# Kernel tuning notes

Hardware: AMD Instinct MI355X
Metric: run time of the kernel (lower is better)

The kernel has to match this reference:

```python
import jax, jax.numpy as jnp
import numpy as np

K = 20          # num neighbors (init kwarg k)
BN_EPS = 1e-5   # PyTorch BatchNorm default eps


def setup_inputs() -> dict:
    key = jax.random.key(0)
    k1, k2 = jax.random.split(key, 2)
    x = jax.random.normal(k1, (8, 64, 4096), dtype=jnp.float32)       # (b, d, n)
    w = jax.random.normal(k2, (64, 128), dtype=jnp.float32) * 0.05    # Conv2d 1x1: (out=64, in=2*64)
    gamma = jnp.ones((64,), jnp.float32)    # BatchNorm1d weight
    beta = jnp.zeros((64,), jnp.float32)    # BatchNorm1d bias
    return {"x": x, "w": w, "gamma": gamma, "beta": beta}


def reference(x, w, gamma, beta):
    # x: (b, d, n)
    xt = jnp.swapaxes(x, 1, 2)                       # (b, n, d)
    # kNN via pairwise squared euclidean distance (same ordering as torch.cdist)
    sq = jnp.sum(xt * xt, axis=-1)                   # (b, n)
    d2 = sq[:, :, None] + sq[:, None, :] - 2.0 * jnp.einsum('bnd,bmd->bnm', xt, xt)
    _, idx = jax.lax.top_k(-d2, K)                   # (b, n, K) smallest distances
    # gather neighbor features: (b, n, K, d)
    nb = jax.vmap(lambda pts, i: pts[i])(xt, idx)
    ctr = xt[:, :, None, :]                          # (b, n, 1, d)
    # edge feature = concat([neighbor - x, x]) -> (b, n, K, 2d)
    feat = jnp.concatenate([nb - ctr, jnp.broadcast_to(ctr, nb.shape)], axis=-1)
    # 1x1 conv (no bias) then max over neighbors
    h = jnp.max(jnp.einsum('bnkc,oc->bnko', feat, w), axis=2)   # (b, n, out)
    # BatchNorm1d (training mode: batch statistics over (b, n), biased var)
    mean = jnp.mean(h, axis=(0, 1))
    var = jnp.mean((h - mean) ** 2, axis=(0, 1))
    hn = (h - mean) / jnp.sqrt(var + BN_EPS) * gamma + beta
    out = jax.nn.gelu(hn, approximate=False)         # exact GELU (PyTorch default)
    return jnp.swapaxes(out, 1, 2)                   # (b, out, n)
```

## Files before the change

### kernel.cpp

```cpp
#include <hip/hip_runtime.h>

#define BIGF 3.402823466e38f

typedef __attribute__((ext_vector_type(8))) short bf16x8;
typedef __attribute__((ext_vector_type(4))) float f32x4;

__device__ __forceinline__ void gload_lds16(const float* g, float* lds) {
  __builtin_amdgcn_global_load_lds((const __attribute__((address_space(1))) void*)g,
                                   (__attribute__((address_space(3))) void*)lds, 16, 0, 0);
}
__device__ __forceinline__ void gload_lds16u(const unsigned short* g, unsigned short* lds) {
  __builtin_amdgcn_global_load_lds((const __attribute__((address_space(1))) void*)g,
                                   (__attribute__((address_space(3))) void*)lds, 16, 0, 0);
}

__device__ __forceinline__ unsigned short bf16_rne(float f) {
  unsigned int u = __float_as_uint(f);
  return (unsigned short)((u + 0x7fffu + ((u >> 16) & 1u)) >> 16);
}

__global__ __launch_bounds__(256) void k1_pre(const float* __restrict__ x, const float* __restrict__ w,
                                              float* __restrict__ sq, float* __restrict__ y,
                                              float* __restrict__ delta, unsigned short* __restrict__ xhl) {
  __shared__ __align__(16) float xt[64][68];
  __shared__ __align__(16) float ws[128][64];
  const int t = threadIdx.x;
  const int bid = blockIdx.x;
  const int b = bid >> 6;
  const int n0 = (bid & 63) << 6;
  const float* xb = x + (size_t)b * 64 * 4096;

#pragma unroll
  for (int rep = 0; rep < 16; ++rep) {
    int id = rep * 256 + t;
    int d = id >> 6, n = id & 63;
    xt[n][d] = xb[(size_t)d * 4096 + n0 + n];
  }
#pragma unroll
  for (int rep = 0; rep < 32; ++rep) {
    int id = rep * 256 + t;
    int u = id >> 6, dd = id & 63;
    ws[u][dd] = w[(u & 63) * 128 + ((u >> 6) << 6) + dd];
  }
  __syncthreads();

  {
    const int p = t >> 2;
    const int cg = t & 3;
    uint4* orow = (uint4*)xhl + ((size_t)(b << 12) + n0 + p) * 16;
#pragma unroll
    for (int cc = 0; cc < 4; ++cc) {
      const int c = cg * 4 + cc;
      const int kb = (c & 7) * 8;
      const bool lohalf = (c >= 8);
      unsigned int pk[4];
#pragma unroll
      for (int j2 = 0; j2 < 4; ++j2) {
        unsigned short u0, u1;
#pragma unroll
        for (int e = 0; e < 2; ++e) {
          const float xv = xt[p][kb + j2 * 2 + e];
          unsigned short h = bf16_rne(xv);
          unsigned short r;
          if (!lohalf) r = h;
          else r = bf16_rne(xv - __uint_as_float(((unsigned int)h) << 16));
          if (e == 0) u0 = r; else u1 = r;
        }
        pk[j2] = (unsigned int)u0 | ((unsigned int)u1 << 16);
      }
      uint4 v;
      v.x = pk[0]; v.y = pk[1]; v.z = pk[2]; v.w = pk[3];
      orow[c ^ (p & 7)] = v;
    }
  }

  const int p = t & 63;
  const int oc = t >> 6;
  float accy[16], accz[16];
#pragma unroll
  for (int j = 0; j < 16; ++j) { accy[j] = 0.f; accz[j] = 0.f; }

#pragma unroll 4
  for (int d4 = 0; d4 < 16; ++d4) {
    const float4 xv = *(const float4*)&xt[p][d4 * 4];
#pragma unroll
    for (int j = 0; j < 16; ++j) {
      const int o = oc * 16 + j;
      const float4 wy = *(const float4*)&ws[o][d4 * 4];
      const float4 wz = *(const float4*)&ws[o + 64][d4 * 4];
      accy[j] = fmaf(xv.x, wy.x, fmaf(xv.y, wy.y, fmaf(xv.z, wy.z, fmaf(xv.w, wy.w, accy[j]))));
      accz[j] = fmaf(xv.x, wz.x, fmaf(xv.y, wz.y, fmaf(xv.z, wz.z, fmaf(xv.w, wz.w, accz[j]))));
    }
  }

  if (oc == 0) {
    float s = 0.f;
#pragma unroll
    for (int d4 = 0; d4 < 16; ++d4) {
      const float4 v = *(const float4*)&xt[p][d4 * 4];
      s = fmaf(v.x, v.x, fmaf(v.y, v.y, fmaf(v.z, v.z, fmaf(v.w, v.w, s))));
    }
    sq[b * 4096 + n0 + p] = s;
  }

  const size_t row = ((size_t)b * 4096 + n0 + p) * 64 + oc * 16;
#pragma unroll
  for (int j4 = 0; j4 < 4; ++j4) {
    float4 yv = make_float4(accy[j4 * 4], accy[j4 * 4 + 1], accy[j4 * 4 + 2], accy[j4 * 4 + 3]);
    float4 dv = make_float4(accz[j4 * 4] - accy[j4 * 4], accz[j4 * 4 + 1] - accy[j4 * 4 + 1],
                            accz[j4 * 4 + 2] - accy[j4 * 4 + 2], accz[j4 * 4 + 3] - accy[j4 * 4 + 3]);
    *(float4*)&y[row + j4 * 4] = yv;
    *(float4*)&delta[row + j4 * 4] = dv;
  }
}

__global__ __launch_bounds__(256, 2) void k2_knn(const unsigned short* __restrict__ xhl,
                                                 const float* __restrict__ sq,
                                                 int* __restrict__ idx_out) {
  __shared__ __align__(16) float smem[4096 + 8192 + 6656 + 256];
  const int t = threadIdx.x;
  const int lane = t & 63;
  const int w = t >> 6;
  float* BsW = smem + 4096 + (w << 11);
  uint4* BsW4 = (uint4*)BsW;
  const uint4* As4 = (const uint4*)smem;
  uint2* bufL = (uint2*)(smem + 12288) + ((w << 6) + lane) * 13;
  volatile float* thrW = smem + 18944;

  const int bid = blockIdx.x;
  const int b = bid >> 6;
  const int n0 = (bid & 63) << 6;
  const int pn = lane & 15, q = lane >> 4;

  const unsigned short* xr = xhl + ((size_t)(b << 12)) * 128;
  const float* sqb = sq + (b << 12);

  thrW[t] = BIGF;

  {
    unsigned short* asu = (unsigned short*)smem;
#pragma unroll
    for (int qq = 0; qq < 4; ++qq) {
      const int kk = w * 4 + qq;
      gload_lds16u(xr + (size_t)n0 * 128 + kk * 512 + lane * 8, asu + kk * 512);
    }
  }
  __syncthreads();

  bf16x8 bfr[4][4];
#pragma unroll
  for (int nt = 0; nt < 4; ++nt)
#pragma unroll
    for (int j = 0; j < 4; ++j)
      bfr[nt][j] = *reinterpret_cast<const bf16x8*>(&As4[((nt << 4) + pn) * 16 + (((j << 2) + q) ^ (pn & 7))]);

  float kd[20];
  int ki[20];
#pragma unroll
  for (int s = 0; s < 20; ++s) { kd[s] = BIGF; ki[s] = -1; }
  const float sqn = sqb[n0 + lane];
  const int myn = lane;
  const int swz = myn & 7;
  int cnt = 0;

  auto ins = [&](float vd, int vi) {
#pragma unroll
    for (int s = 0; s < 20; ++s) {
      const float od = kd[s];
      const int oi = ki[s];
      const bool lt = vd < od;
      kd[s] = lt ? vd : od;
      ki[s] = lt ? vi : oi;
      vd = lt ? od : vd;
      vi = lt ? oi : vi;
    }
  };

  auto drain = [&]() {
#pragma unroll 1
    for (int j = 0; j < 12; ++j) {
      if (!__any(j < cnt)) break;
      if (j < cnt) {
        const uint2 e = bufL[j];
        const float dv = __uint_as_float(e.x);
        if (dv < kd[19]) ins(dv, (int)e.y);
      }
    }
    cnt = 0;
    thrW[(myn << 2) + w] = kd[19];
  };

  const f32x4 zero4 = {0.f, 0.f, 0.f, 0.f};
  f32x4 acc[4][2];
#pragma unroll
  for (int nt = 0; nt < 4; ++nt) { acc[nt][0] = zero4; acc[nt][1] = zero4; }

  for (int kt = 0; kt < 32; ++kt) {
    const int mbase = (w + 4 * kt) << 5;
    {
      unsigned short* bsu = (unsigned short*)BsW;
      const unsigned short* src = xr + (size_t)mbase * 128;
#pragma unroll
      for (int k = 0; k < 8; ++k) gload_lds16u(src + k * 512 + lane * 8, bsu + k * 512);
    }
    const f32x4 sqm0 = *(const f32x4*)&sqb[mbase + (q << 2)];
    const f32x4 sqm1 = *(const f32x4*)&sqb[mbase + 16 + (q << 2)];

    const float tw0 = thrW[(myn << 2) + 0];
    const float tw1 = thrW[(myn << 2) + 1];
    const float tw2 = thrW[(myn << 2) + 2];
    const float tw3 = thrW[(myn << 2) + 3];
    float thrS = fminf(fminf(tw0, tw1), fminf(tw2, tw3));
    thrS = fminf(thrS, kd[19]);
    const float thr2 = (thrS - sqn) + 0.0625f;

    __builtin_amdgcn_s_waitcnt(0x0F70);

#pragma unroll
    for (int mt = 0; mt < 2; ++mt) {
      bf16x8 afr[4];
#pragma unroll
      for (int j = 0; j < 4; ++j)
        afr[j] = *reinterpret_cast<const bf16x8*>(&BsW4[((mt << 4) + pn) * 16 + (((j << 2) + q) ^ (pn & 7))]);
#pragma unroll
      for (int nt = 0; nt < 4; ++nt) {
        f32x4 a = acc[nt][mt];
        a = __builtin_amdgcn_mfma_f32_16x16x32_bf16(afr[0], bfr[nt][0], a, 0, 0, 0);
        a = __builtin_amdgcn_mfma_f32_16x16x32_bf16(afr[1], bfr[nt][1], a, 0, 0, 0);
        a = __builtin_amdgcn_mfma_f32_16x16x32_bf16(afr[0], bfr[nt][2], a, 0, 0, 0);
        a = __builtin_amdgcn_mfma_f32_16x16x32_bf16(afr[1], bfr[nt][3], a, 0, 0, 0);
        a = __builtin_amdgcn_mfma_f32_16x16x32_bf16(afr[2], bfr[nt][0], a, 0, 0, 0);
        a = __builtin_amdgcn_mfma_f32_16x16x32_bf16(afr[3], bfr[nt][1], a, 0, 0, 0);
        acc[nt][mt] = a;
      }
    }

#pragma unroll
    for (int nt = 0; nt < 4; ++nt) {
#pragma unroll
      for (int mt = 0; mt < 2; ++mt) {
        const int n = (nt << 4) + pn;
        const int g = (mt << 2) + q;
        const int pc = g ^ (n & 7);
        const f32x4 sv = mt ? sqm1 : sqm0;
        f32x4 dv = sv - 2.0f * acc[nt][mt];
        *(f32x4*)&BsW[(n << 5) + (pc << 2)] = dv;
        acc[nt][mt] = zero4;
      }
    }

#pragma unroll 1
    for (int half = 0; half < 2; ++half) {
      const int cb = half << 2;
      const float4 v0 = *(const float4*)&BsW[(myn << 5) + (((cb + 0) ^ swz) << 2)];
      const float4 v1 = *(const float4*)&BsW[(myn << 5) + (((cb + 1) ^ swz) << 2)];
      const float4 v2 = *(const float4*)&BsW[(myn << 5) + (((cb + 2) ^ swz) << 2)];
      const float4 v3 = *(const float4*)&BsW[(myn << 5) + (((cb + 3) ^ swz) << 2)];
#pragma unroll
      for (int cc = 0; cc < 4; ++cc) {
        const float4 v = (cc == 0) ? v0 : (cc == 1) ? v1 : (cc == 2) ? v2 : v3;
        const int mb = mbase + ((cb + cc) << 2);
        const float mn = fminf(fminf(v.x, v.y), fminf(v.z, v.w));
        if (mn < thr2) {
          if (v.x < thr2) { bufL[cnt] = make_uint2(__float_as_uint(sqn + v.x), (unsigned)mb); cnt++; }
          if (v.y < thr2) { bufL[cnt] = make_uint2(__float_as_uint(sqn + v.y), (unsigned)(mb + 1)); cnt++; }
          if (v.z < thr2) { bufL[cnt] = make_uint2(__float_as_uint(sqn + v.z), (unsigned)(mb + 2)); cnt++; }
          if (v.w < thr2) { bufL[cnt] = make_uint2(__float_as_uint(sqn + v.w), (unsigned)(mb + 3)); cnt++; }
        }
        if (__any(cnt > 8)) drain();
      }
    }
  }
  drain();

  __syncthreads();
  float* pf = smem;
  int* pi = (int*)(smem + 5120);
#pragma unroll
  for (int s = 0; s < 20; ++s) {
    pf[(w * 20 + s) * 64 + lane] = kd[s];
    pi[(w * 20 + s) * 64 + lane] = ki[s];
  }
  __syncthreads();
  if (w == 0) {
    auto insTie = [&](float vd, int vi) {
#pragma unroll
      for (int s = 0; s < 20; ++s) {
        const float od = kd[s];
        const int oi = ki[s];
        const bool lt = (vd < od) || (vd == od && vi < oi);
        kd[s] = lt ? vd : od;
        ki[s] = lt ? vi : oi;
        vd = lt ? od : vd;
        vi = lt ? oi : vi;
      }
    };
    for (int ww = 1; ww < 4; ++ww) {
#pragma unroll 1
      for (int s = 0; s < 20; ++s) {
        const float dv = pf[(ww * 20 + s) * 64 + lane];
        const int iv = pi[(ww * 20 + s) * 64 + lane];
        if (dv < kd[19] || (dv == kd[19] && iv < ki[19])) insTie(dv, iv);
      }
    }
    int* orow = idx_out + ((size_t)(b << 12) + n0 + lane) * 20;
#pragma unroll
    for (int s = 0; s < 20; ++s) orow[s] = ki[s];
  }
}

__global__ __launch_bounds__(256) void k3_gather(const float* __restrict__ y,
                                                 const float* __restrict__ delta,
                                                 const int* __restrict__ idx,
                                                 float* __restrict__ h,
                                                 float* __restrict__ sums,
                                                 float* __restrict__ sumsq) {
  const int t = threadIdx.x;
  const int lane = t & 63;
  const int w = t >> 6;
  const int blk = blockIdx.x;
  float s1 = 0.f, s2 = 0.f;
  for (int p = 0; p < 16; ++p) {
    const int ng = blk * 64 + w * 16 + p;
    const int b = ng >> 12;
    const int* row = idx + (size_t)ng * 20;
    float mx = -BIGF;
#pragma unroll
    for (int kk = 0; kk < 20; ++kk) {
      const int nbr = row[kk];
      mx = fmaxf(mx, y[((size_t)(b << 12) + nbr) * 64 + lane]);
    }
    const float hv = mx + delta[(size_t)ng * 64 + lane];
    h[(size_t)ng * 64 + lane] = hv;
    s1 += hv;
    s2 += hv * hv;
  }
  __shared__ float r1[4][64], r2[4][64];
  r1[w][lane] = s1;
  r2[w][lane] = s2;
  __syncthreads();
  if (w == 0) {
    const float a = r1[0][lane] + r1[1][lane] + r1[2][lane] + r1[3][lane];
    const float c = r2[0][lane] + r2[1][lane] + r2[2][lane] + r2[3][lane];
    atomicAdd(&sums[lane], a);
    atomicAdd(&sumsq[lane], c);
  }
}

__global__ __launch_bounds__(256) void k4_bn(const float* __restrict__ h,
                                             const float* __restrict__ sums,
                                             const float* __restrict__ sumsq,
                                             const float* __restrict__ gamma,
                                             const float* __restrict__ beta,
                                             float* __restrict__ out) {
  __shared__ float tile[64][65];
  const int bid = blockIdx.x;
  const int b = bid >> 6;
  const int n0 = (bid & 63) << 6;
  const int t = threadIdx.x;
  const int o = t & 63;
#pragma unroll
  for (int it = 0; it < 16; ++it) {
    const int n = (t >> 6) * 16 + it;
    tile[n][o] = h[(((size_t)b << 12) + n0 + n) * 64 + o];
  }
  __syncthreads();
  const int j = t & 63;
#pragma unroll
  for (int it = 0; it < 16; ++it) {
    const int oo = (t >> 6) * 16 + it;
    const float mean = sums[oo] * (1.0f / 32768.0f);
    const float var = sumsq[oo] * (1.0f / 32768.0f) - mean * mean;
    const float sc = gamma[oo] / sqrtf(var + 1e-5f);
    const float hv = tile[j][oo];
    const float hn = (hv - mean) * sc + beta[oo];
    const float g = 0.5f * hn * (1.0f + erff(hn * 0.70710678118654752f));
    out[((size_t)(b * 64 + oo)) * 4096 + n0 + j] = g;
  }
}

extern "C" void kernel_launch(void* const* d_in, const int* in_sizes, int n_in,
                              void* d_out, int out_size, void* d_ws, size_t ws_size,
                              hipStream_t stream) {
  const float* x = (const float*)d_in[0];
  const float* w = (const float*)d_in[1];
  const float* gamma = (const float*)d_in[2];
  const float* beta = (const float*)d_in[3];
  float* out = (float*)d_out;

  float* sq_ws = (float*)d_ws;
  float* y_ws = sq_ws + 32768;
  float* delta_ws = y_ws + 2097152;
  float* h_ws = delta_ws + 2097152;
  int* idx_ws = (int*)(h_ws + 2097152);
  float* sums = (float*)(idx_ws + 655360);
  float* sumsq = sums + 64;
  unsigned short* xhl = (unsigned short*)h_ws;

  hipMemsetAsync(sums, 0, 2 * 64 * sizeof(float), stream);
  k1_pre<<<512, 256, 0, stream>>>(x, w, sq_ws, y_ws, delta_ws, xhl);
  k2_knn<<<512, 256, 0, stream>>>(xhl, sq_ws, idx_ws);
  k3_gather<<<512, 256, 0, stream>>>(y_ws, delta_ws, idx_ws, h_ws, sums, sumsq);
  k4_bn<<<512, 256, 0, stream>>>(h_ws, sums, sumsq, gamma, beta, out);
}
```

Before: 344.2 us.

## Shrink kNN LDS footprint, share threshold via atomicMin, tighten candidate margin

The per-thread candidate buffer moves from an interleaved uint2 array into two strided arrays (distance, index) that reuse the A-tile region after the B fragments are loaded into registers. This cuts k2_knn shared memory from about 19.2K floats to 12.35K floats, which may allow more resident blocks. The four per-wave threshold slots become one shared threshold per point updated with atomicMin on the float bit pattern. The threshold is refreshed after each drain, the drain trigger drops to more than 4 entries, and the pruning margin shrinks from 0.0625 to 0.001. The smaller margin prunes more aggressively, so bf16 rounding error in the distances could drop true neighbours.

Result: slower. 352.8 us (+2.5%).

```diff
diff --git a/kernel.cpp b/kernel.cpp
--- a/kernel.cpp
+++ b/kernel.cpp
@@ -5,10 +5,6 @@
 typedef __attribute__((ext_vector_type(8))) short bf16x8;
 typedef __attribute__((ext_vector_type(4))) float f32x4;
 
-__device__ __forceinline__ void gload_lds16(const float* g, float* lds) {
-  __builtin_amdgcn_global_load_lds((const __attribute__((address_space(1))) void*)g,
-                                   (__attribute__((address_space(3))) void*)lds, 16, 0, 0);
-}
 __device__ __forceinline__ void gload_lds16u(const unsigned short* g, unsigned short* lds) {
   __builtin_amdgcn_global_load_lds((const __attribute__((address_space(1))) void*)g,
                                    (__attribute__((address_space(3))) void*)lds, 16, 0, 0);
@@ -117,25 +113,29 @@
 __global__ __launch_bounds__(256, 2) void k2_knn(const unsigned short* __restrict__ xhl,
                                                  const float* __restrict__ sq,
                                                  int* __restrict__ idx_out) {
-  __shared__ __align__(16) float smem[4096 + 8192 + 6656 + 256];
+  __shared__ __align__(16) float smem[12352];
   const int t = threadIdx.x;
   const int lane = t & 63;
   const int w = t >> 6;
   float* BsW = smem + 4096 + (w << 11);
   uint4* BsW4 = (uint4*)BsW;
   const uint4* As4 = (const uint4*)smem;
-  uint2* bufL = (uint2*)(smem + 12288) + ((w << 6) + lane) * 13;
-  volatile float* thrW = smem + 18944;
+  unsigned* bufD = (unsigned*)smem;
+  unsigned* bufI = (unsigned*)(smem + 2048);
+  unsigned* thrNa = (unsigned*)(smem + 12288);
+  volatile unsigned* thrNv = (volatile unsigned*)(smem + 12288);
 
   const int bid = blockIdx.x;
   const int b = bid >> 6;
   const int n0 = (bid & 63) << 6;
   const int pn = lane & 15, q = lane >> 4;
+  const int myn = lane;
+  const int swz = myn & 7;
 
   const unsigned short* xr = xhl + ((size_t)(b << 12)) * 128;
   const float* sqb = sq + (b << 12);
 
-  thrW[t] = BIGF;
+  if (t < 64) thrNa[t] = 0x7F7FFFFFu;
 
   {
     unsigned short* asu = (unsigned short*)smem;
@@ -145,6 +145,8 @@
       gload_lds16u(xr + (size_t)n0 * 128 + kk * 512 + lane * 8, asu + kk * 512);
     }
   }
+  const float sqn = sqb[n0 + myn];
+  __builtin_amdgcn_s_waitcnt(0x0F70);
   __syncthreads();
 
   bf16x8 bfr[4][4];
@@ -153,14 +155,12 @@
 #pragma unroll
     for (int j = 0; j < 4; ++j)
       bfr[nt][j] = *reinterpret_cast<const bf16x8*>(&As4[((nt << 4) + pn) * 16 + (((j << 2) + q) ^ (pn & 7))]);
+  __syncthreads();
 
   float kd[20];
   int ki[20];
 #pragma unroll
   for (int s = 0; s < 20; ++s) { kd[s] = BIGF; ki[s] = -1; }
-  const float sqn = sqb[n0 + lane];
-  const int myn = lane;
-  const int swz = myn & 7;
   int cnt = 0;
 
   auto ins = [&](float vd, int vi) {
@@ -178,16 +178,16 @@
 
   auto drain = [&]() {
 #pragma unroll 1
-    for (int j = 0; j < 12; ++j) {
+    for (int j = 0; j < 8; ++j) {
       if (!__any(j < cnt)) break;
       if (j < cnt) {
-        const uint2 e = bufL[j];
-        const float dv = __uint_as_float(e.x);
-        if (dv < kd[19]) ins(dv, (int)e.y);
+        const float dv = __uint_as_float(bufD[j * 256 + t]);
+        const int iv = (int)bufI[j * 256 + t];
+        if (dv < kd[19]) ins(dv, iv);
       }
     }
     cnt = 0;
-    thrW[(myn << 2) + w] = kd[19];
+    atomicMin(&thrNa[myn], __float_as_uint(kd[19]));
   };
 
   const f32x4 zero4 = {0.f, 0.f, 0.f, 0.f};
@@ -205,16 +205,9 @@
     }
     const f32x4 sqm0 = *(const f32x4*)&sqb[mbase + (q << 2)];
     const f32x4 sqm1 = *(const f32x4*)&sqb[mbase + 16 + (q << 2)];
-
-    const float tw0 = thrW[(myn << 2) + 0];
-    const float tw1 = thrW[(myn << 2) + 1];
-    const float tw2 = thrW[(myn << 2) + 2];
-    const float tw3 = thrW[(myn << 2) + 3];
-    float thrS = fminf(fminf(tw0, tw1), fminf(tw2, tw3));
-    thrS = fminf(thrS, kd[19]);
-    const float thr2 = (thrS - sqn) + 0.0625f;
-
     __builtin_amdgcn_s_waitcnt(0x0F70);
+
+    float thr2 = (fminf(__uint_as_float(thrNv[myn]), kd[19]) - sqn) + 0.001f;
 
 #pragma unroll
     for (int mt = 0; mt < 2; ++mt) {
@@ -262,12 +255,15 @@
         const int mb = mbase + ((cb + cc) << 2);
         const float mn = fminf(fminf(v.x, v.y), fminf(v.z, v.w));
         if (mn < thr2) {
-          if (v.x < thr2) { bufL[cnt] = make_uint2(__float_as_uint(sqn + v.x), (unsigned)mb); cnt++; }
-          if (v.y < thr2) { bufL[cnt] = make_uint2(__float_as_uint(sqn + v.y), (unsigned)(mb + 1)); cnt++; }
-          if (v.z < thr2) { bufL[cnt] = make_uint2(__float_as_uint(sqn + v.z), (unsigned)(mb + 2)); cnt++; }
-          if (v.w < thr2) { bufL[cnt] = make_uint2(__float_as_uint(sqn + v.w), (unsigned)(mb + 3)); cnt++; }
+          if (v.x < thr2) { bufD[cnt * 256 + t] = __float_as_uint(sqn + v.x); bufI[cnt * 256 + t] = (unsigned)mb; cnt++; }
+          if (v.y < thr2) { bufD[cnt * 256 + t] = __float_as_uint(sqn + v.y); bufI[cnt * 256 + t] = (unsigned)(mb + 1); cnt++; }
+          if (v.z < thr2) { bufD[cnt * 256 + t] = __float_as_uint(sqn + v.z); bufI[cnt * 256 + t] = (unsigned)(mb + 2); cnt++; }
+          if (v.w < thr2) { bufD[cnt * 256 + t] = __float_as_uint(sqn + v.w); bufI[cnt * 256 + t] = (unsigned)(mb + 3); cnt++; }
         }
-        if (__any(cnt > 8)) drain();
+        if (__any(cnt > 4)) {
+          drain();
+          thr2 = fminf(thr2, (fminf(__uint_as_float(thrNv[myn]), kd[19]) - sqn) + 0.001f);
+        }
       }
     }
   }
```
